# Kernel tuning notes

Hardware: AMD Instinct MI355X
Metric: run time of the kernel (lower is better)

## Reference

```python
import jax, jax.numpy as jnp
import numpy as np

S_DIM = 8      # state_dim
O_DIM = 4      # obs_dim
HID = (S_DIM * S_DIM + O_DIM * O_DIM) * 10   # 800
BATCH = 128
SEQ = 32
NS = 16        # num_samples
P_DROP = 0.2
DROP_KEY = jax.random.key(42)

def f_dyn(x):
    # synthetic nonlinear dynamics (stand-in for system_model.f, vmapped over batch)
    return 0.9 * x + 0.1 * jnp.sin(x)

def h_obs(x):
    # synthetic nonlinear observation (stand-in for system_model.h)
    return jnp.tanh(x[..., :O_DIM])

def l2_normalize(x, eps=1e-12):
    # matches torch F.normalize(p=2, dim=1): x / max(||x||, eps)
    n = jnp.linalg.norm(x, axis=-1, keepdims=True)
    return x / jnp.maximum(n, eps)

def setup_inputs() -> dict:
    key = jax.random.key(0)
    ks = jax.random.split(key, 8)
    g = 0.02
    return {
        "y_seq": jax.random.normal(ks[0], (BATCH, SEQ, O_DIM), dtype=jnp.float32),
        "W1": jax.random.normal(ks[1], (HID, S_DIM + O_DIM), dtype=jnp.float32) * g,
        "b1": jnp.zeros((HID,), jnp.float32),
        "W_ih": jax.random.normal(ks[2], (3 * HID, HID), dtype=jnp.float32) * g,
        "W_hh": jax.random.normal(ks[3], (3 * HID, HID), dtype=jnp.float32) * g,
        "b_ih": jnp.zeros((3 * HID,), jnp.float32),
        "b_hh": jnp.zeros((3 * HID,), jnp.float32),
        "W_out": jax.random.normal(ks[4], (S_DIM * O_DIM, HID), dtype=jnp.float32) * g,
        "b_out": jnp.zeros((S_DIM * O_DIM,), jnp.float32),
        "num_samples": NS,
    }

def _forward(y_seq, W1, b1, W_ih, W_hh, b_ih, b_hh, W_out, b_out, num_samples):
    B = y_seq.shape[0]
    keep = 1.0 - P_DROP

    def gru_cell(x, h):
        # torch nn.GRU single-step math; x,h: [..., HID]
        gi = x @ W_ih.T + b_ih
        gh = h @ W_hh.T + b_hh
        gi_r, gi_z, gi_n = jnp.split(gi, 3, axis=-1)
        gh_r, gh_z, gh_n = jnp.split(gh, 3, axis=-1)
        r = jax.nn.sigmoid(gi_r + gh_r)
        z = jax.nn.sigmoid(gi_z + gh_z)
        n = jnp.tanh(gi_n + r * gh_n)
        return (1.0 - z) * n + z * h

    def step(carry, inp):
        x_prev, dx_prev, h_ens = carry            # [B,S], [B,S], [NS,B,HID]
        y_t, t = inp
        x_pred = f_dyn(x_prev)                    # [B,S] (same for every sample j)
        y_hat = h_obs(x_pred)                     # [B,O]
        innov = y_t - y_hat                       # [B,O]
        nn_in = jnp.concatenate([l2_normalize(dx_prev), l2_normalize(innov)], axis=-1)
        a = jax.nn.relu(nn_in @ W1.T + b1)        # [B,HID]
        k1, k2 = jax.random.split(jax.random.fold_in(DROP_KEY, t))
        m1 = jax.random.bernoulli(k1, keep, (num_samples, B, HID)).astype(a.dtype)
        a_ens = a[None] * m1 / keep               # MC-dropout per ensemble member
        h_new = gru_cell(a_ens, h_ens)            # [NS,B,HID] (vectorized over samples)
        K_vec = h_new @ W_out.T + b_out           # [NS,B,S*O]
        m2 = jax.random.bernoulli(k2, keep, K_vec.shape).astype(a.dtype)
        K = (K_vec * m2 / keep).reshape(num_samples, B, S_DIM, O_DIM)
        ens = x_pred[None] + jnp.einsum('jbso,bo->jbs', K, innov)  # [NS,B,S]
        x_filt = ens.mean(axis=0)                 # [B,S]
        diff = ens - x_filt[None]                 # [NS,B,S]
        P_filt = jnp.einsum('jbs,jbt->bst', diff, diff) / num_samples
        dx = x_filt - x_pred                      # delta_x_prev = x_filt - f(x_prev)
        return (x_filt, dx, h_new), (x_filt, P_filt)

    x0 = jnp.zeros((B, S_DIM), y_seq.dtype)
    dx0 = jnp.zeros((B, S_DIM), y_seq.dtype)
    h0 = jnp.zeros((num_samples, B, HID), y_seq.dtype)
    ts = jnp.arange(y_seq.shape[1])
    _, (xs, Ps) = jax.lax.scan(step, (x0, dx0, h0), (jnp.swapaxes(y_seq, 0, 1), ts))
    # xs: [T,B,S] -> [B,T,S]; Ps: [T,B,S,S] -> [B,T,S,S]
    return jnp.swapaxes(xs, 0, 1), jnp.swapaxes(Ps, 0, 1)

def reference(y_seq, W1, b1, W_ih, W_hh, b_ih, b_hh, W_out, b_out, num_samples):
    return _forward(y_seq, W1, b1, W_ih, W_hh, b_ih, b_hh, W_out, b_out, num_samples)
```

## Files before the change

kernel.cpp:

```cpp
#include <hip/hip_runtime.h>
#include <stdint.h>

#define NSAMP 16
#define BATCH 128
#define SEQLEN 32
#define SDIM 8
#define ODIM 4
#define HID 800
#define MROWS (NSAMP * BATCH)
#define KEEPP 0.8f

typedef __attribute__((ext_vector_type(8))) short short8v;
typedef __attribute__((ext_vector_type(4))) float float4v;

__host__ __device__ __forceinline__ void tf2x32(uint32_t k0, uint32_t k1,
                                                uint32_t x0, uint32_t x1,
                                                uint32_t& o0, uint32_t& o1) {
  uint32_t ks2 = k0 ^ k1 ^ 0x1BD11BDAu;
  x0 += k0; x1 += k1;
#define TFR(r) { x0 += x1; x1 = (x1 << (r)) | (x1 >> (32 - (r))); x1 ^= x0; }
  TFR(13) TFR(15) TFR(26) TFR(6)
  x0 += k1; x1 += ks2 + 1u;
  TFR(17) TFR(29) TFR(16) TFR(24)
  x0 += ks2; x1 += k0 + 2u;
  TFR(13) TFR(15) TFR(26) TFR(6)
  x0 += k0; x1 += k1 + 3u;
  TFR(17) TFR(29) TFR(16) TFR(24)
  x0 += k1; x1 += ks2 + 4u;
  TFR(13) TFR(15) TFR(26) TFR(6)
  x0 += ks2; x1 += k0 + 5u;
#undef TFR
  o0 = x0; o1 = x1;
}

__device__ __forceinline__ float bits_to_unit(uint32_t bits) {
  return __uint_as_float((bits >> 9) | 0x3F800000u) - 1.0f;
}

__device__ __forceinline__ float tf_uniform_part(uint32_t k0, uint32_t k1, uint32_t idx) {
  uint32_t b1, b2;
  tf2x32(k0, k1, 0u, idx, b1, b2);
  return bits_to_unit(b1 ^ b2);
}

__device__ __forceinline__ ushort f2bf(float f) {
  uint32_t u = __float_as_uint(f);
  uint32_t r = (u + 0x7FFFu + ((u >> 16) & 1u)) >> 16;
  return (ushort)r;
}

__device__ __forceinline__ void bar_sync() {
  __builtin_amdgcn_sched_barrier(0);
  __builtin_amdgcn_s_barrier();
  __builtin_amdgcn_sched_barrier(0);
}

__global__ void convert_w_kernel(const float* __restrict__ W_ih, const float* __restrict__ W_hh,
                                 ushort* __restrict__ Wib, ushort* __restrict__ Whb) {
  int i = (blockIdx.x * 256 + threadIdx.x) * 4;
  if (i >= 2400 * HID) return;
  float4 v1 = *reinterpret_cast<const float4*>(W_ih + i);
  float4 v2 = *reinterpret_cast<const float4*>(W_hh + i);
  ushort4 o1, o2;
  o1.x = f2bf(v1.x); o1.y = f2bf(v1.y); o1.z = f2bf(v1.z); o1.w = f2bf(v1.w);
  o2.x = f2bf(v2.x); o2.y = f2bf(v2.y); o2.z = f2bf(v2.z); o2.w = f2bf(v2.w);
  *reinterpret_cast<ushort4*>(Wib + i) = o1;
  *reinterpret_cast<ushort4*>(Whb + i) = o2;
}

__global__ void transpose_wout_kernel(const float* __restrict__ W_out, float* __restrict__ WoutT) {
  int i = blockIdx.x * 256 + threadIdx.x;
  if (i < 32 * HID) {
    int o = i / HID, k = i - o * HID;
    WoutT[k * 32 + o] = W_out[i];
  }
}

__global__ void a_ens_kernel(const float* __restrict__ a, ushort* __restrict__ aeb,
                             uint32_t k0, uint32_t k1) {
  int base = (blockIdx.x * blockDim.x + threadIdx.x) * 4;
  if (base >= MROWS * HID) return;
  int row = base / HID;
  int b = row % BATCH;
  int col = base - row * HID;
  float4 av = *reinterpret_cast<const float4*>(a + b * HID + col);
  ushort4 ov;
#pragma unroll
  for (int q = 0; q < 4; ++q) {
    float u = tf_uniform_part(k0, k1, (uint32_t)(base + q));
    float f = (&av.x)[q] * ((u < KEEPP) ? 1.25f : 0.0f);
    (&ov.x)[q] = f2bf(f);
  }
  *reinterpret_cast<ushort4*>(aeb + base) = ov;
}

#define LDSBUF 28672

__global__ __launch_bounds__(256, 2) void gru_mfma_kernel(
    const ushort* __restrict__ aeb, const ushort* __restrict__ hb,
    const ushort* __restrict__ Wib, const ushort* __restrict__ Whb,
    const float* __restrict__ h_old,
    const float* __restrict__ b_ih, const float* __restrict__ b_hh,
    float* __restrict__ h_new, ushort* __restrict__ h_new_b) {
  __shared__ __align__(1024) char lds[2 * LDSBUF];

  const int tid = threadIdx.x;
  const int wid = tid >> 6;
  const int lane = tid & 63;
  const int m0 = blockIdx.x * 128;
  const int n0 = blockIdx.y * 32;

  float4v acc[6][2][2];
#pragma unroll
  for (int g = 0; g < 6; ++g)
#pragma unroll
    for (int mf = 0; mf < 2; ++mf)
#pragma unroll
      for (int nf = 0; nf < 2; ++nf)
        acc[g][mf][nf] = (float4v)(0.0f);

  const int rlo = lane >> 2;
  const int sslot = (lane & 3) ^ ((lane >> 3) & 3);
  const int kg = lane >> 4;
  const int l15 = lane & 15;

  const ushort* gp[7];
  int ldso[7];
#pragma unroll
  for (int s = 0; s < 7; ++s) {
    int i = s * 4 + wid;
    if (i < 16) {
      int src = i >> 3, i8 = i & 7;
      ldso[s] = src * 8192 + i8 * 1024;
      const ushort* base = src ? hb : aeb;
      gp[s] = base + (size_t)(m0 + i8 * 16 + rlo) * HID + sslot * 8;
    } else {
      int j = i - 16, g = j >> 1, half = j & 1;
      ldso[s] = 16384 + g * 2048 + half * 1024;
      const ushort* base = (g < 3) ? Wib : Whb;
      int wrow = n0 + (g % 3) * HID + half * 16 + rlo;
      gp[s] = base + (size_t)wrow * HID + sslot * 8;
    }
  }

#define STAGE(BUF) do {                                                          \
    _Pragma("unroll")                                                            \
    for (int s = 0; s < 7; ++s) {                                                \
      __builtin_amdgcn_global_load_lds(                                          \
          (const __attribute__((address_space(1))) void*)gp[s],                  \
          (__attribute__((address_space(3))) void*)(lds + (BUF)*LDSBUF + ldso[s]),\
          16, 0, 0);                                                             \
      gp[s] += 32;                                                               \
    }                                                                            \
  } while (0)

#define COMPUTE(BUF) do {                                                        \
    const char* lb = lds + (BUF)*LDSBUF;                                         \
    short8v bfr[6][2];                                                           \
    _Pragma("unroll")                                                            \
    for (int g = 0; g < 6; ++g)                                                  \
      _Pragma("unroll")                                                          \
      for (int nf = 0; nf < 2; ++nf) {                                           \
        int row = nf * 16 + l15;                                                 \
        int off = 16384 + g * 2048 + row * 64 + ((kg ^ ((row >> 1) & 3)) << 4);  \
        bfr[g][nf] = *reinterpret_cast<const short8v*>(lb + off);                \
      }                                                                          \
    short8v afr[2][2];                                                           \
    _Pragma("unroll")                                                            \
    for (int src = 0; src < 2; ++src)                                            \
      _Pragma("unroll")                                                          \
      for (int mf = 0; mf < 2; ++mf) {                                           \
        int row = wid * 32 + mf * 16 + l15;                                      \
        int off = src * 8192 + row * 64 + ((kg ^ ((row >> 1) & 3)) << 4);        \
        afr[src][mf] = *reinterpret_cast<const short8v*>(lb + off);              \
      }                                                                          \
    _Pragma("unroll")                                                            \
    for (int g = 0; g < 6; ++g) {                                                \
      const int src = (g < 3) ? 0 : 1;                                           \
      _Pragma("unroll")                                                          \
      for (int mf = 0; mf < 2; ++mf)                                             \
        _Pragma("unroll")                                                        \
        for (int nf = 0; nf < 2; ++nf)                                           \
          acc[g][mf][nf] = __builtin_amdgcn_mfma_f32_16x16x32_bf16(              \
              afr[src][mf], bfr[g][nf], acc[g][mf][nf], 0, 0, 0);                \
    }                                                                            \
  } while (0)

  STAGE(0);
#pragma unroll 1
  for (int k = 0; k < 24; k += 2) {
    STAGE(1);
    asm volatile("s_waitcnt vmcnt(7)" ::: "memory");
    bar_sync();
    COMPUTE(0);
    bar_sync();
    STAGE(0);
    asm volatile("s_waitcnt vmcnt(7)" ::: "memory");
    bar_sync();
    COMPUTE(1);
    bar_sync();
  }
  asm volatile("s_waitcnt vmcnt(0)" ::: "memory");
  bar_sync();
  COMPUTE(0);

  const int rowq = (lane >> 4) * 4;
#pragma unroll
  for (int nf = 0; nf < 2; ++nf) {
    const int col = n0 + nf * 16 + l15;
    const float bir = b_ih[col], biz = b_ih[col + HID], bin = b_ih[col + 2 * HID];
    const float bhr = b_hh[col], bhz = b_hh[col + HID], bhn = b_hh[col + 2 * HID];
#pragma unroll
    for (int mf = 0; mf < 2; ++mf) {
#pragma unroll
      for (int reg = 0; reg < 4; ++reg) {
        const int m = m0 + wid * 32 + mf * 16 + rowq + reg;
        float gir = acc[0][mf][nf][reg] + bir;
        float giz = acc[1][mf][nf][reg] + biz;
        float gin = acc[2][mf][nf][reg] + bin;
        float ghr = acc[3][mf][nf][reg] + bhr;
        float ghz = acc[4][mf][nf][reg] + bhz;
        float ghn = acc[5][mf][nf][reg] + bhn;
        float r = 1.0f / (1.0f + expf(-(gir + ghr)));
        float z = 1.0f / (1.0f + expf(-(giz + ghz)));
        float nval = tanhf(gin + r * ghn);
        float hv = h_old[(size_t)m * HID + col];
        float res = (1.0f - z) * nval + z * hv;
        h_new[(size_t)m * HID + col] = res;
        h_new_b[(size_t)m * HID + col] = f2bf(res);
      }
    }
  }
#undef STAGE
#undef COMPUTE
}

__global__ void kvec_ens_kernel(const float* __restrict__ h_new,
                                const float* __restrict__ WoutT,
                                const float* __restrict__ b_out,
                                const float* __restrict__ x_pred,
                                const float* __restrict__ innov,
                                float* __restrict__ ens,
                                uint32_t k0, uint32_t k1) {
  const int jb = blockIdx.x;
  const int b = jb & (BATCH - 1);
  const int tid = threadIdx.x;
  const int o = tid & 31;
  const int kk = tid >> 5;

  const float* hrow = h_new + (size_t)jb * HID;
  float partial = 0.0f;
  for (int k = kk * 100; k < kk * 100 + 100; ++k)
    partial = fmaf(hrow[k], WoutT[k * 32 + o], partial);

  __shared__ float red[8][32];
  __shared__ float Kv[32];
  red[kk][o] = partial;
  __syncthreads();
  if (tid < 32) {
    float s = 0.0f;
#pragma unroll
    for (int q = 0; q < 8; ++q) s += red[q][tid];
    s += b_out[tid];
    float u = tf_uniform_part(k0, k1, (uint32_t)(jb * 32 + tid));
    Kv[tid] = (u < KEEPP) ? s * 1.25f : 0.0f;
  }
  __syncthreads();
  if (tid < SDIM) {
    float s = x_pred[b * SDIM + tid];
#pragma unroll
    for (int oo = 0; oo < ODIM; ++oo)
      s = fmaf(Kv[tid * ODIM + oo], innov[b * ODIM + oo], s);
    ens[jb * SDIM + tid] = s;
  }
}

__global__ void reduce_prep_kernel(const float* __restrict__ ens,
                                   float* __restrict__ x_pred,
                                   float* __restrict__ innov,
                                   const float* __restrict__ y_seq,
                                   const float* __restrict__ W1,
                                   const float* __restrict__ b1,
                                   float* __restrict__ a,
                                   float* __restrict__ out_xs, float* __restrict__ out_Ps,
                                   int t) {
  const int b = blockIdx.x;
  const int tid = threadIdx.x;
  __shared__ float e[NSAMP][SDIM];
  __shared__ float xf[SDIM];
  __shared__ float dxs[SDIM];
  __shared__ float xpn[SDIM];
  __shared__ float inv[ODIM];
  __shared__ float nin[SDIM + ODIM];

  if (t >= 0) {
    if (tid < NSAMP * SDIM) {
      int j = tid >> 3, s = tid & 7;
      e[j][s] = ens[(j * BATCH + b) * SDIM + s];
    }
    __syncthreads();
    if (tid < SDIM) {
      float s = 0.0f;
#pragma unroll
      for (int j = 0; j < NSAMP; ++j) s += e[j][tid];
      s *= (1.0f / NSAMP);
      xf[tid] = s;
      out_xs[(b * SEQLEN + t) * SDIM + tid] = s;
      dxs[tid] = s - x_pred[b * SDIM + tid];
    }
    __syncthreads();
    if (tid < SDIM * SDIM) {
      int s = tid >> 3, u = tid & 7;
      float accv = 0.0f;
#pragma unroll
      for (int j = 0; j < NSAMP; ++j)
        accv += (e[j][s] - xf[s]) * (e[j][u] - xf[u]);
      out_Ps[((b * SEQLEN + t) * SDIM + s) * SDIM + u] = accv * (1.0f / NSAMP);
    }
  } else {
    if (tid < SDIM) { xf[tid] = 0.0f; dxs[tid] = 0.0f; }
  }
  if (t == SEQLEN - 1) return;
  __syncthreads();
  if (tid < SDIM) {
    float x = xf[tid];
    float xp = 0.9f * x + 0.1f * sinf(x);
    xpn[tid] = xp;
    x_pred[b * SDIM + tid] = xp;
  }
  __syncthreads();
  if (tid < ODIM) {
    float yh = tanhf(xpn[tid]);
    float iv = y_seq[(b * SEQLEN + (t + 1)) * ODIM + tid] - yh;
    inv[tid] = iv;
    innov[b * ODIM + tid] = iv;
  }
  __syncthreads();
  if (tid == 0) {
    float nd = 0.0f;
    for (int s = 0; s < SDIM; ++s) nd += dxs[s] * dxs[s];
    nd = fmaxf(sqrtf(nd), 1e-12f);
    for (int s = 0; s < SDIM; ++s) nin[s] = dxs[s] / nd;
    float ni = 0.0f;
    for (int o2 = 0; o2 < ODIM; ++o2) ni += inv[o2] * inv[o2];
    ni = fmaxf(sqrtf(ni), 1e-12f);
    for (int o2 = 0; o2 < ODIM; ++o2) nin[SDIM + o2] = inv[o2] / ni;
  }
  __syncthreads();
  for (int i = tid; i < HID; i += blockDim.x) {
    float s = b1[i];
#pragma unroll
    for (int c = 0; c < 12; ++c) s = fmaf(nin[c], W1[i * 12 + c], s);
    a[b * HID + i] = fmaxf(s, 0.0f);
  }
}

extern "C" void kernel_launch(void* const* d_in, const int* in_sizes, int n_in,
                              void* d_out, int out_size, void* d_ws, size_t ws_size,
                              hipStream_t stream) {
  (void)in_sizes; (void)n_in; (void)out_size; (void)ws_size;
  const float* y_seq = (const float*)d_in[0];
  const float* W1 = (const float*)d_in[1];
  const float* b1 = (const float*)d_in[2];
  const float* W_ih = (const float*)d_in[3];
  const float* W_hh = (const float*)d_in[4];
  const float* b_ih = (const float*)d_in[5];
  const float* b_hh = (const float*)d_in[6];
  const float* W_out = (const float*)d_in[7];
  const float* b_out = (const float*)d_in[8];

  char* ws = (char*)d_ws;
  size_t off = 0;
  float* h_a = (float*)(ws + off);    off += (size_t)MROWS * HID * 4;
  float* h_b = (float*)(ws + off);    off += (size_t)MROWS * HID * 4;
  ushort* hb_a = (ushort*)(ws + off); off += (size_t)MROWS * HID * 2;
  ushort* hb_b = (ushort*)(ws + off); off += (size_t)MROWS * HID * 2;
  ushort* aeb = (ushort*)(ws + off);  off += (size_t)MROWS * HID * 2;
  ushort* Wib = (ushort*)(ws + off);  off += (size_t)2400 * HID * 2;
  ushort* Whb = (ushort*)(ws + off);  off += (size_t)2400 * HID * 2;
  float* a_buf = (float*)(ws + off);  off += (size_t)BATCH * HID * 4;
  float* WoutT = (float*)(ws + off);  off += (size_t)HID * 32 * 4;
  float* x_pred = (float*)(ws + off); off += (size_t)BATCH * SDIM * 4;
  float* innov = (float*)(ws + off);  off += (size_t)BATCH * ODIM * 4;
  float* ens = (float*)(ws + off);    off += (size_t)NSAMP * BATCH * SDIM * 4;

  float* out_xs = (float*)d_out;
  float* out_Ps = out_xs + (size_t)BATCH * SEQLEN * SDIM;

  hipMemsetAsync(h_a, 0, (size_t)MROWS * HID * 4, stream);
  hipMemsetAsync(hb_a, 0, (size_t)MROWS * HID * 2, stream);
  convert_w_kernel<<<1875, 256, 0, stream>>>(W_ih, W_hh, Wib, Whb);
  transpose_wout_kernel<<<100, 256, 0, stream>>>(W_out, WoutT);
  reduce_prep_kernel<<<BATCH, 256, 0, stream>>>(ens, x_pred, innov, y_seq, W1, b1,
                                                a_buf, out_xs, out_Ps, -1);

  float* hc = h_a;  float* hn = h_b;
  ushort* hcb = hb_a; ushort* hnb = hb_b;
  dim3 gg(MROWS / 128, HID / 32);
  for (int t = 0; t < SEQLEN; ++t) {
    uint32_t kt0, kt1, k1a, k1b, k2a, k2b;
    tf2x32(0u, 42u, 0u, (uint32_t)t, kt0, kt1);
    tf2x32(kt0, kt1, 0u, 0u, k1a, k1b);
    tf2x32(kt0, kt1, 0u, 1u, k2a, k2b);

    a_ens_kernel<<<1600, 256, 0, stream>>>(a_buf, aeb, k1a, k1b);
    gru_mfma_kernel<<<gg, 256, 0, stream>>>(aeb, hcb, Wib, Whb, hc, b_ih, b_hh, hn, hnb);
    kvec_ens_kernel<<<MROWS, 256, 0, stream>>>(hn, WoutT, b_out, x_pred, innov, ens, k2a, k2b);
    reduce_prep_kernel<<<BATCH, 256, 0, stream>>>(ens, x_pred, innov, y_seq, W1, b1,
                                                  a_buf, out_xs, out_Ps, t);
    float* tmp = hc; hc = hn; hn = tmp;
    ushort* tmpb = hcb; hcb = hnb; hnb = tmpb;
  }
}
```

Before: 1.882 ms.

## Load GRU A operands directly into registers and remap blocks per XCD

The ensemble-input and hidden-state A fragments are now read straight from global memory into registers, one set per stage and double-buffered, instead of being staged through LDS. Only the weight B tiles still go through LDS, which shrinks the shared buffer from 56 KB to 24 KB. The launch grid becomes 1D, and the block index is remapped so that each of the 8 XCDs handles two M-blocks across all N-blocks, meant to improve L2 reuse of the A rows. The cost is more register pressure and less coalesced global reads for A, with 64-byte contiguous segments per row.

```diff
diff --git a/kernel.cpp b/kernel.cpp
--- a/kernel.cpp
+++ b/kernel.cpp
@@ -94,7 +94,7 @@
   *reinterpret_cast<ushort4*>(aeb + base) = ov;
 }
 
-#define LDSBUF 28672
+#define LDSB 12288
 
 __global__ __launch_bounds__(256, 2) void gru_mfma_kernel(
     const ushort* __restrict__ aeb, const ushort* __restrict__ hb,
@@ -102,13 +102,19 @@
     const float* __restrict__ h_old,
     const float* __restrict__ b_ih, const float* __restrict__ b_hh,
     float* __restrict__ h_new, ushort* __restrict__ h_new_b) {
-  __shared__ __align__(1024) char lds[2 * LDSBUF];
+  __shared__ __align__(1024) char lds[2 * LDSB];
 
   const int tid = threadIdx.x;
   const int wid = tid >> 6;
   const int lane = tid & 63;
-  const int m0 = blockIdx.x * 128;
-  const int n0 = blockIdx.y * 32;
+
+  const int bid = blockIdx.x;
+  const int xcd = bid & 7;
+  const int q = bid >> 3;
+  const int mm = q / 25;
+  const int nblk = q - mm * 25;
+  const int m0 = (xcd * 2 + mm) * 128;
+  const int n0 = nblk * 32;
 
   float4v acc[6][2][2];
 #pragma unroll
@@ -124,55 +130,59 @@
   const int kg = lane >> 4;
   const int l15 = lane & 15;
 
-  const ushort* gp[7];
-  int ldso[7];
-#pragma unroll
-  for (int s = 0; s < 7; ++s) {
+  const ushort* gp[3];
+  int ldso[3];
+#pragma unroll
+  for (int s = 0; s < 3; ++s) {
     int i = s * 4 + wid;
-    if (i < 16) {
-      int src = i >> 3, i8 = i & 7;
-      ldso[s] = src * 8192 + i8 * 1024;
-      const ushort* base = src ? hb : aeb;
-      gp[s] = base + (size_t)(m0 + i8 * 16 + rlo) * HID + sslot * 8;
-    } else {
-      int j = i - 16, g = j >> 1, half = j & 1;
-      ldso[s] = 16384 + g * 2048 + half * 1024;
-      const ushort* base = (g < 3) ? Wib : Whb;
-      int wrow = n0 + (g % 3) * HID + half * 16 + rlo;
-      gp[s] = base + (size_t)wrow * HID + sslot * 8;
-    }
-  }
-
-#define STAGE(BUF) do {                                                          \
+    int g = i >> 1, half = i & 1;
+    ldso[s] = g * 2048 + half * 1024;
+    const ushort* base = (g < 3) ? Wib : Whb;
+    int wrow = n0 + (g % 3) * HID + half * 16 + rlo;
+    gp[s] = base + (size_t)wrow * HID + sslot * 8;
+  }
+
+  const ushort* ap[2][2];
+#pragma unroll
+  for (int mf = 0; mf < 2; ++mf) {
+    const int row = m0 + wid * 32 + mf * 16 + l15;
+    ap[0][mf] = aeb + (size_t)row * HID + kg * 8;
+    ap[1][mf] = hb + (size_t)row * HID + kg * 8;
+  }
+
+  short8v ar0[2][2], ar1[2][2];
+
+#define STAGE_B(BUF) do {                                                        \
     _Pragma("unroll")                                                            \
-    for (int s = 0; s < 7; ++s) {                                                \
+    for (int s = 0; s < 3; ++s) {                                                \
       __builtin_amdgcn_global_load_lds(                                          \
           (const __attribute__((address_space(1))) void*)gp[s],                  \
-          (__attribute__((address_space(3))) void*)(lds + (BUF)*LDSBUF + ldso[s]),\
+          (__attribute__((address_space(3))) void*)(lds + (BUF)*LDSB + ldso[s]), \
           16, 0, 0);                                                             \
       gp[s] += 32;                                                               \
     }                                                                            \
   } while (0)
 
-#define COMPUTE(BUF) do {                                                        \
-    const char* lb = lds + (BUF)*LDSBUF;                                         \
+#define LOAD_A(SET) do {                                                         \
+    _Pragma("unroll")                                                            \
+    for (int s2 = 0; s2 < 2; ++s2)                                               \
+      _Pragma("unroll")                                                          \
+      for (int mf = 0; mf < 2; ++mf) {                                           \
+        SET[s2][mf] = *reinterpret_cast<const short8v*>(ap[s2][mf]);             \
+        ap[s2][mf] += 32;                                                        \
+      }                                                                          \
+  } while (0)
+
+#define COMPUTE(BUF, SET) do {                                                   \
+    const char* lb = lds + (BUF)*LDSB;                                           \
     short8v bfr[6][2];                                                           \
     _Pragma("unroll")                                                            \
     for (int g = 0; g < 6; ++g)                                                  \
       _Pragma("unroll")                                                          \
       for (int nf = 0; nf < 2; ++nf) {                                           \
         int row = nf * 16 + l15;                                                 \
-        int off = 16384 + g * 2048 + row * 64 + ((kg ^ ((row >> 1) & 3)) << 4);  \
+        int off = g * 2048 + row * 64 + ((kg ^ ((row >> 1) & 3)) << 4);          \
         bfr[g][nf] = *reinterpret_cast<const short8v*>(lb + off);                \
-      }                                                                          \
-    short8v afr[2][2];                                                           \
-    _Pragma("unroll")                                                            \
-    for (int src = 0; src < 2; ++src)                                            \
-      _Pragma("unroll")                                                          \
-      for (int mf = 0; mf < 2; ++mf) {                                           \
-        int row = wid * 32 + mf * 16 + l15;                                      \
-        int off = src * 8192 + row * 64 + ((kg ^ ((row >> 1) & 3)) << 4);        \
-        afr[src][mf] = *reinterpret_cast<const short8v*>(lb + off);              \
       }                                                                          \
     _Pragma("unroll")                                                            \
     for (int g = 0; g < 6; ++g) {                                                \
@@ -182,27 +192,30 @@
         _Pragma("unroll")                                                        \
         for (int nf = 0; nf < 2; ++nf)                                           \
           acc[g][mf][nf] = __builtin_amdgcn_mfma_f32_16x16x32_bf16(              \
-              afr[src][mf], bfr[g][nf], acc[g][mf][nf], 0, 0, 0);                \
+              SET[src][mf], bfr[g][nf], acc[g][mf][nf], 0, 0, 0);                \
     }                                                                            \
   } while (0)
 
-  STAGE(0);
+  STAGE_B(0);
+  LOAD_A(ar0);
 #pragma unroll 1
   for (int k = 0; k < 24; k += 2) {
-    STAGE(1);
+    STAGE_B(1);
+    LOAD_A(ar1);
     asm volatile("s_waitcnt vmcnt(7)" ::: "memory");
     bar_sync();
-    COMPUTE(0);
+    COMPUTE(0, ar0);
     bar_sync();
-    STAGE(0);
+    STAGE_B(0);
+    LOAD_A(ar0);
     asm volatile("s_waitcnt vmcnt(7)" ::: "memory");
     bar_sync();
-    COMPUTE(1);
+    COMPUTE(1, ar1);
     bar_sync();
   }
   asm volatile("s_waitcnt vmcnt(0)" ::: "memory");
   bar_sync();
-  COMPUTE(0);
+  COMPUTE(0, ar0);
 
   const int rowq = (lane >> 4) * 4;
 #pragma unroll
@@ -231,7 +244,8 @@
       }
     }
   }
-#undef STAGE
+#undef STAGE_B
+#undef LOAD_A
 #undef COMPUTE
 }
 
@@ -396,7 +410,6 @@
 
   float* hc = h_a;  float* hn = h_b;
   ushort* hcb = hb_a; ushort* hnb = hb_b;
-  dim3 gg(MROWS / 128, HID / 32);
   for (int t = 0; t < SEQLEN; ++t) {
     uint32_t kt0, kt1, k1a, k1b, k2a, k2b;
     tf2x32(0u, 42u, 0u, (uint32_t)t, kt0, kt1);
@@ -404,7 +417,7 @@
     tf2x32(kt0, kt1, 0u, 1u, k2a, k2b);
 
     a_ens_kernel<<<1600, 256, 0, stream>>>(a_buf, aeb, k1a, k1b);
-    gru_mfma_kernel<<<gg, 256, 0, stream>>>(aeb, hcb, Wib, Whb, hc, b_ih, b_hh, hn, hnb);
+    gru_mfma_kernel<<<400, 256, 0, stream>>>(aeb, hcb, Wib, Whb, hc, b_ih, b_hh, hn, hnb);
     kvec_ens_kernel<<<MROWS, 256, 0, stream>>>(hn, WoutT, b_out, x_pred, innov, ens, k2a, k2b);
     reduce_prep_kernel<<<BATCH, 256, 0, stream>>>(ens, x_pred, innov, y_seq, W1, b1,
                                                   a_buf, out_xs, out_Ps, t);
```

New measurement: 2.087 ms. +10.9%, slower.

## Shrink GRU GEMM N-tile to 16, remap blocks per XCD, raise occupancy

Applied to the files above, without the earlier changes.

The GRU gate GEMM tile width drops from 32 to 16 columns. The grid becomes 1D with 800 blocks, mapped so that each XCD (block id mod 8) handles two fixed 128-row M tiles, which should keep the A/H rows resident in that XCD's L2. The smaller tile cuts LDS and register use, allowing 3 blocks per CU, and s_setprio is raised around the MFMA sequence. In exchange, each weight column tile now feeds fewer MFMAs per A-fragment load, so the kernel does more global and LDS traffic per flop.

```diff
diff --git a/kernel.cpp b/kernel.cpp
--- a/kernel.cpp
+++ b/kernel.cpp
@@ -94,9 +94,9 @@
   *reinterpret_cast<ushort4*>(aeb + base) = ov;
 }
 
-#define LDSBUF 28672
-
-__global__ __launch_bounds__(256, 2) void gru_mfma_kernel(
+#define LDSBUF 22528
+
+__global__ __launch_bounds__(256, 3) void gru_mfma_kernel(
     const ushort* __restrict__ aeb, const ushort* __restrict__ hb,
     const ushort* __restrict__ Wib, const ushort* __restrict__ Whb,
     const float* __restrict__ h_old,
@@ -107,45 +107,50 @@
   const int tid = threadIdx.x;
   const int wid = tid >> 6;
   const int lane = tid & 63;
-  const int m0 = blockIdx.x * 128;
-  const int n0 = blockIdx.y * 32;
-
-  float4v acc[6][2][2];
+
+  const int bid = blockIdx.x;
+  const int xcd = bid & 7;
+  const int q = bid >> 3;
+  const int mloc = q / 50;
+  const int nblk = q - mloc * 50;
+  const int m0 = (xcd * 2 + mloc) * 128;
+  const int n0 = nblk * 16;
+
+  float4v acc[6][2];
 #pragma unroll
   for (int g = 0; g < 6; ++g)
 #pragma unroll
     for (int mf = 0; mf < 2; ++mf)
-#pragma unroll
-      for (int nf = 0; nf < 2; ++nf)
-        acc[g][mf][nf] = (float4v)(0.0f);
+      acc[g][mf] = (float4v)(0.0f);
 
   const int rlo = lane >> 2;
   const int sslot = (lane & 3) ^ ((lane >> 3) & 3);
   const int kg = lane >> 4;
   const int l15 = lane & 15;
 
-  const ushort* gp[7];
-  int ldso[7];
-#pragma unroll
-  for (int s = 0; s < 7; ++s) {
+  const ushort* gp[6];
+  int ldso[6];
+#pragma unroll
+  for (int s = 0; s < 6; ++s) {
     int i = s * 4 + wid;
+    if (i >= 22) i -= 22;
     if (i < 16) {
       int src = i >> 3, i8 = i & 7;
       ldso[s] = src * 8192 + i8 * 1024;
       const ushort* base = src ? hb : aeb;
       gp[s] = base + (size_t)(m0 + i8 * 16 + rlo) * HID + sslot * 8;
     } else {
-      int j = i - 16, g = j >> 1, half = j & 1;
-      ldso[s] = 16384 + g * 2048 + half * 1024;
+      int g = i - 16;
+      ldso[s] = 16384 + g * 1024;
       const ushort* base = (g < 3) ? Wib : Whb;
-      int wrow = n0 + (g % 3) * HID + half * 16 + rlo;
+      int wrow = n0 + (g % 3) * HID + rlo;
       gp[s] = base + (size_t)wrow * HID + sslot * 8;
     }
   }
 
 #define STAGE(BUF) do {                                                          \
     _Pragma("unroll")                                                            \
-    for (int s = 0; s < 7; ++s) {                                                \
+    for (int s = 0; s < 6; ++s) {                                                \
       __builtin_amdgcn_global_load_lds(                                          \
           (const __attribute__((address_space(1))) void*)gp[s],                  \
           (__attribute__((address_space(3))) void*)(lds + (BUF)*LDSBUF + ldso[s]),\
@@ -156,15 +161,12 @@
 
 #define COMPUTE(BUF) do {                                                        \
     const char* lb = lds + (BUF)*LDSBUF;                                         \
-    short8v bfr[6][2];                                                           \
+    short8v bfr[6];                                                              \
     _Pragma("unroll")                                                            \
-    for (int g = 0; g < 6; ++g)                                                  \
-      _Pragma("unroll")                                                          \
-      for (int nf = 0; nf < 2; ++nf) {                                           \
-        int row = nf * 16 + l15;                                                 \
-        int off = 16384 + g * 2048 + row * 64 + ((kg ^ ((row >> 1) & 3)) << 4);  \
-        bfr[g][nf] = *reinterpret_cast<const short8v*>(lb + off);                \
-      }                                                                          \
+    for (int g = 0; g < 6; ++g) {                                                \
+      int off = 16384 + g * 1024 + l15 * 64 + ((kg ^ ((l15 >> 1) & 3)) << 4);    \
+      bfr[g] = *reinterpret_cast<const short8v*>(lb + off);                      \
+    }                                                                            \
     short8v afr[2][2];                                                           \
     _Pragma("unroll")                                                            \
     for (int src = 0; src < 2; ++src)                                            \
@@ -174,28 +176,28 @@
         int off = src * 8192 + row * 64 + ((kg ^ ((row >> 1) & 3)) << 4);        \
         afr[src][mf] = *reinterpret_cast<const short8v*>(lb + off);              \
       }                                                                          \
+    __builtin_amdgcn_s_setprio(1);                                               \
     _Pragma("unroll")                                                            \
     for (int g = 0; g < 6; ++g) {                                                \
       const int src = (g < 3) ? 0 : 1;                                           \
       _Pragma("unroll")                                                          \
       for (int mf = 0; mf < 2; ++mf)                                             \
-        _Pragma("unroll")                                                        \
-        for (int nf = 0; nf < 2; ++nf)                                           \
-          acc[g][mf][nf] = __builtin_amdgcn_mfma_f32_16x16x32_bf16(              \
-              afr[src][mf], bfr[g][nf], acc[g][mf][nf], 0, 0, 0);                \
+        acc[g][mf] = __builtin_amdgcn_mfma_f32_16x16x32_bf16(                    \
+            afr[src][mf], bfr[g], acc[g][mf], 0, 0, 0);                          \
     }                                                                            \
+    __builtin_amdgcn_s_setprio(0);                                               \
   } while (0)
 
   STAGE(0);
 #pragma unroll 1
   for (int k = 0; k < 24; k += 2) {
     STAGE(1);
-    asm volatile("s_waitcnt vmcnt(7)" ::: "memory");
+    asm volatile("s_waitcnt vmcnt(6)" ::: "memory");
     bar_sync();
     COMPUTE(0);
     bar_sync();
     STAGE(0);
-    asm volatile("s_waitcnt vmcnt(7)" ::: "memory");
+    asm volatile("s_waitcnt vmcnt(6)" ::: "memory");
     bar_sync();
     COMPUTE(1);
     bar_sync();
@@ -205,30 +207,27 @@
   COMPUTE(0);
 
   const int rowq = (lane >> 4) * 4;
-#pragma unroll
-  for (int nf = 0; nf < 2; ++nf) {
-    const int col = n0 + nf * 16 + l15;
-    const float bir = b_ih[col], biz = b_ih[col + HID], bin = b_ih[col + 2 * HID];
-    const float bhr = b_hh[col], bhz = b_hh[col + HID], bhn = b_hh[col + 2 * HID];
-#pragma unroll
-    for (int mf = 0; mf < 2; ++mf) {
-#pragma unroll
-      for (int reg = 0; reg < 4; ++reg) {
-        const int m = m0 + wid * 32 + mf * 16 + rowq + reg;
-        float gir = acc[0][mf][nf][reg] + bir;
-        float giz = acc[1][mf][nf][reg] + biz;
-        float gin = acc[2][mf][nf][reg] + bin;
-        float ghr = acc[3][mf][nf][reg] + bhr;
-        float ghz = acc[4][mf][nf][reg] + bhz;
-        float ghn = acc[5][mf][nf][reg] + bhn;
-        float r = 1.0f / (1.0f + expf(-(gir + ghr)));
-        float z = 1.0f / (1.0f + expf(-(giz + ghz)));
-        float nval = tanhf(gin + r * ghn);
-        float hv = h_old[(size_t)m * HID + col];
-        float res = (1.0f - z) * nval + z * hv;
-        h_new[(size_t)m * HID + col] = res;
-        h_new_b[(size_t)m * HID + col] = f2bf(res);
-      }
+  const int col = n0 + l15;
+  const float bir = b_ih[col], biz = b_ih[col + HID], bin = b_ih[col + 2 * HID];
+  const float bhr = b_hh[col], bhz = b_hh[col + HID], bhn = b_hh[col + 2 * HID];
+#pragma unroll
+  for (int mf = 0; mf < 2; ++mf) {
+#pragma unroll
+    for (int reg = 0; reg < 4; ++reg) {
+      const int m = m0 + wid * 32 + mf * 16 + rowq + reg;
+      float gir = acc[0][mf][reg] + bir;
+      float giz = acc[1][mf][reg] + biz;
+      float gin = acc[2][mf][reg] + bin;
+      float ghr = acc[3][mf][reg] + bhr;
+      float ghz = acc[4][mf][reg] + bhz;
+      float ghn = acc[5][mf][reg] + bhn;
+      float r = 1.0f / (1.0f + expf(-(gir + ghr)));
+      float z = 1.0f / (1.0f + expf(-(giz + ghz)));
+      float nval = tanhf(gin + r * ghn);
+      float hv = h_old[(size_t)m * HID + col];
+      float res = (1.0f - z) * nval + z * hv;
+      h_new[(size_t)m * HID + col] = res;
+      h_new_b[(size_t)m * HID + col] = f2bf(res);
     }
   }
 #undef STAGE
@@ -396,7 +395,6 @@
 
   float* hc = h_a;  float* hn = h_b;
   ushort* hcb = hb_a; ushort* hnb = hb_b;
-  dim3 gg(MROWS / 128, HID / 32);
   for (int t = 0; t < SEQLEN; ++t) {
     uint32_t kt0, kt1, k1a, k1b, k2a, k2b;
     tf2x32(0u, 42u, 0u, (uint32_t)t, kt0, kt1);
@@ -404,7 +402,7 @@
     tf2x32(kt0, kt1, 0u, 1u, k2a, k2b);
 
     a_ens_kernel<<<1600, 256, 0, stream>>>(a_buf, aeb, k1a, k1b);
-    gru_mfma_kernel<<<gg, 256, 0, stream>>>(aeb, hcb, Wib, Whb, hc, b_ih, b_hh, hn, hnb);
+    gru_mfma_kernel<<<800, 256, 0, stream>>>(aeb, hcb, Wib, Whb, hc, b_ih, b_hh, hn, hnb);
     kvec_ens_kernel<<<MROWS, 256, 0, stream>>>(hn, WoutT, b_out, x_pred, innov, ens, k2a, k2b);
     reduce_prep_kernel<<<BATCH, 256, 0, stream>>>(ens, x_pred, innov, y_seq, W1, b1,
                                                   a_buf, out_xs, out_Ps, t);
```

Result: slower. 2.402 ms (+27.6%).

## Drop fp32 hidden state; take old h from LDS bf16 tile in GRU kernel

Applied to the files above, without the earlier changes.

Removes the fp32 copy of the GRU hidden state. The GEMM kernel now captures the previous h value for its output tile from the bf16 h tile already staged in LDS, at the k-step that matches its column block. The Wout projection kernel reads the bf16 hidden state instead of fp32. This cuts global traffic by dropping one fp32 read and one fp32 write of the 2048x800 state per step, plus a memset, at the cost of carrying h and the z*h blend in bf16 precision.

```diff
diff --git a/kernel.cpp b/kernel.cpp
--- a/kernel.cpp
+++ b/kernel.cpp
@@ -49,6 +49,10 @@
   return (ushort)r;
 }
 
+__device__ __forceinline__ float bf2f(ushort u) {
+  return __uint_as_float((uint32_t)u << 16);
+}
+
 __device__ __forceinline__ void bar_sync() {
   __builtin_amdgcn_sched_barrier(0);
   __builtin_amdgcn_s_barrier();
@@ -99,16 +103,15 @@
 __global__ __launch_bounds__(256, 2) void gru_mfma_kernel(
     const ushort* __restrict__ aeb, const ushort* __restrict__ hb,
     const ushort* __restrict__ Wib, const ushort* __restrict__ Whb,
-    const float* __restrict__ h_old,
     const float* __restrict__ b_ih, const float* __restrict__ b_hh,
-    float* __restrict__ h_new, ushort* __restrict__ h_new_b) {
+    ushort* __restrict__ h_new_b) {
   __shared__ __align__(1024) char lds[2 * LDSBUF];
-
   const int tid = threadIdx.x;
   const int wid = tid >> 6;
   const int lane = tid & 63;
   const int m0 = blockIdx.x * 128;
-  const int n0 = blockIdx.y * 32;
+  const int by = blockIdx.y;
+  const int n0 = by * 32;
 
   float4v acc[6][2][2];
 #pragma unroll
@@ -123,6 +126,7 @@
   const int sslot = (lane & 3) ^ ((lane >> 3) & 3);
   const int kg = lane >> 4;
   const int l15 = lane & 15;
+  const int rowq = (lane >> 4) * 4;
 
   const ushort* gp[7];
   int ldso[7];
@@ -143,6 +147,8 @@
     }
   }
 
+  ushort hsnap[2][2][4];
+
 #define STAGE(BUF) do {                                                          \
     _Pragma("unroll")                                                            \
     for (int s = 0; s < 7; ++s) {                                                \
@@ -152,6 +158,21 @@
           16, 0, 0);                                                             \
       gp[s] += 32;                                                               \
     }                                                                            \
+  } while (0)
+
+#define SNAP(BUF) do {                                                           \
+    _Pragma("unroll")                                                            \
+    for (int mf = 0; mf < 2; ++mf)                                               \
+      _Pragma("unroll")                                                          \
+      for (int nf = 0; nf < 2; ++nf)                                             \
+        _Pragma("unroll")                                                        \
+        for (int reg = 0; reg < 4; ++reg) {                                      \
+          int rr = wid * 32 + mf * 16 + rowq + reg;                              \
+          int kk = nf * 16 + l15;                                                \
+          int off = (BUF) * LDSBUF + 8192 + rr * 64 +                            \
+                    ((((kk >> 3) ^ ((rr >> 1) & 3))) << 4) + (kk & 7) * 2;       \
+          hsnap[mf][nf][reg] = *reinterpret_cast<const ushort*>(lds + off);      \
+        }                                                                        \
   } while (0)
 
 #define COMPUTE(BUF) do {                                                        \
@@ -192,19 +213,21 @@
     STAGE(1);
     asm volatile("s_waitcnt vmcnt(7)" ::: "memory");
     bar_sync();
+    if (k == by) SNAP(0);
     COMPUTE(0);
     bar_sync();
     STAGE(0);
     asm volatile("s_waitcnt vmcnt(7)" ::: "memory");
     bar_sync();
+    if (k + 1 == by) SNAP(1);
     COMPUTE(1);
     bar_sync();
   }
   asm volatile("s_waitcnt vmcnt(0)" ::: "memory");
   bar_sync();
+  if (by == 24) SNAP(0);
   COMPUTE(0);
 
-  const int rowq = (lane >> 4) * 4;
 #pragma unroll
   for (int nf = 0; nf < 2; ++nf) {
     const int col = n0 + nf * 16 + l15;
@@ -224,18 +247,18 @@
         float r = 1.0f / (1.0f + expf(-(gir + ghr)));
         float z = 1.0f / (1.0f + expf(-(giz + ghz)));
         float nval = tanhf(gin + r * ghn);
-        float hv = h_old[(size_t)m * HID + col];
+        float hv = bf2f(hsnap[mf][nf][reg]);
         float res = (1.0f - z) * nval + z * hv;
-        h_new[(size_t)m * HID + col] = res;
         h_new_b[(size_t)m * HID + col] = f2bf(res);
       }
     }
   }
 #undef STAGE
+#undef SNAP
 #undef COMPUTE
 }
 
-__global__ void kvec_ens_kernel(const float* __restrict__ h_new,
+__global__ void kvec_ens_kernel(const ushort* __restrict__ hnb,
                                 const float* __restrict__ WoutT,
                                 const float* __restrict__ b_out,
                                 const float* __restrict__ x_pred,
@@ -248,10 +271,11 @@
   const int o = tid & 31;
   const int kk = tid >> 5;
 
-  const float* hrow = h_new + (size_t)jb * HID;
+  const ushort* hrow = hnb + (size_t)jb * HID + kk * 100;
+  const float* wc = WoutT + kk * 100 * 32 + o;
   float partial = 0.0f;
-  for (int k = kk * 100; k < kk * 100 + 100; ++k)
-    partial = fmaf(hrow[k], WoutT[k * 32 + o], partial);
+  for (int k = 0; k < 100; ++k)
+    partial = fmaf(bf2f(hrow[k]), wc[k * 32], partial);
 
   __shared__ float red[8][32];
   __shared__ float Kv[32];
@@ -371,8 +395,6 @@
 
   char* ws = (char*)d_ws;
   size_t off = 0;
-  float* h_a = (float*)(ws + off);    off += (size_t)MROWS * HID * 4;
-  float* h_b = (float*)(ws + off);    off += (size_t)MROWS * HID * 4;
   ushort* hb_a = (ushort*)(ws + off); off += (size_t)MROWS * HID * 2;
   ushort* hb_b = (ushort*)(ws + off); off += (size_t)MROWS * HID * 2;
   ushort* aeb = (ushort*)(ws + off);  off += (size_t)MROWS * HID * 2;
@@ -387,14 +409,12 @@
   float* out_xs = (float*)d_out;
   float* out_Ps = out_xs + (size_t)BATCH * SEQLEN * SDIM;
 
-  hipMemsetAsync(h_a, 0, (size_t)MROWS * HID * 4, stream);
   hipMemsetAsync(hb_a, 0, (size_t)MROWS * HID * 2, stream);
   convert_w_kernel<<<1875, 256, 0, stream>>>(W_ih, W_hh, Wib, Whb);
   transpose_wout_kernel<<<100, 256, 0, stream>>>(W_out, WoutT);
   reduce_prep_kernel<<<BATCH, 256, 0, stream>>>(ens, x_pred, innov, y_seq, W1, b1,
                                                 a_buf, out_xs, out_Ps, -1);
 
-  float* hc = h_a;  float* hn = h_b;
   ushort* hcb = hb_a; ushort* hnb = hb_b;
   dim3 gg(MROWS / 128, HID / 32);
   for (int t = 0; t < SEQLEN; ++t) {
@@ -404,11 +424,10 @@
     tf2x32(kt0, kt1, 0u, 1u, k2a, k2b);
 
     a_ens_kernel<<<1600, 256, 0, stream>>>(a_buf, aeb, k1a, k1b);
-    gru_mfma_kernel<<<gg, 256, 0, stream>>>(aeb, hcb, Wib, Whb, hc, b_ih, b_hh, hn, hnb);
-    kvec_ens_kernel<<<MROWS, 256, 0, stream>>>(hn, WoutT, b_out, x_pred, innov, ens, k2a, k2b);
+    gru_mfma_kernel<<<gg, 256, 0, stream>>>(aeb, hcb, Wib, Whb, b_ih, b_hh, hnb);
+    kvec_ens_kernel<<<MROWS, 256, 0, stream>>>(hnb, WoutT, b_out, x_pred, innov, ens, k2a, k2b);
     reduce_prep_kernel<<<BATCH, 256, 0, stream>>>(ens, x_pred, innov, y_seq, W1, b1,
                                                   a_buf, out_xs, out_Ps, t);
-    float* tmp = hc; hc = hn; hn = tmp;
     ushort* tmpb = hcb; hcb = hnb; hnb = tmpb;
   }
 }
```

New measurement: 1.703 ms. -9.5%, faster.
